# Optimization experiments

Hardware: AMD Instinct MI355X
Metric: run time of the kernel (lower is better)

## Reference

```python
import jax, jax.numpy as jnp
import numpy as np

B = 16          # number of point clouds in the batch
PTS = 32768     # points per cloud (lengths sum to N)
N = B * PTS     # total stacked points
D = 512         # feature dim


def setup_inputs() -> dict:
    key = jax.random.key(0)
    k_feat, = jax.random.split(key, 1)
    features = jax.random.normal(k_feat, (N, D), dtype=jnp.float32)
    # per-cloud point counts; must sum to N (static). Equal lengths here,
    # but reference() handles arbitrary ragged lengths.
    stack_lengths = jnp.full((B,), PTS, dtype=jnp.int32)
    return {"stack_lengths": stack_lengths, "features": features}


def reference(stack_lengths, features):
    # Ragged per-segment mean pooling: features [N, D] -> [B, D]
    n_points = features.shape[0]
    batch = stack_lengths.shape[0]
    # segment id for every point; total_repeat_length keeps shapes static under jit
    seg_ids = jnp.repeat(jnp.arange(batch), stack_lengths,
                         total_repeat_length=n_points)
    sums = jax.ops.segment_sum(features, seg_ids, num_segments=batch)  # [B, D]
    counts = stack_lengths.astype(features.dtype)[:, None]             # [B, 1]
    return sums / counts
```

## Files before the change

kernel.cpp:

```cpp
#include <hip/hip_runtime.h>


#define SPLIT 256
#define TPB   128

__global__ void zero_out_kernel(float* __restrict__ out, int n) {
    int i = blockIdx.x * blockDim.x + threadIdx.x;
    if (i < n) out[i] = 0.0f;
}

__global__ __launch_bounds__(TPB) void seg_mean_kernel(
        const int* __restrict__ lens,
        const float* __restrict__ feat,
        float* __restrict__ out,
        int B) {
    const int D = 512;
    const int seg   = blockIdx.x / SPLIT;
    const int split = blockIdx.x % SPLIT;

    long long start = 0;
    for (int b = 0; b < seg; ++b) start += lens[b];
    const int len = lens[seg];

    const int col = threadIdx.x * 4;
    const float* base = feat + start * (long long)D + col;

    float4 acc = make_float4(0.f, 0.f, 0.f, 0.f);
    for (int r = split; r < len; r += SPLIT) {
        float4 v = *(const float4*)(base + (long long)r * D);
        acc.x += v.x; acc.y += v.y; acc.z += v.z; acc.w += v.w;
    }

    const float inv = (len > 0) ? (1.0f / (float)len) : 0.0f;
    float* o = out + (long long)seg * D + col;
    atomicAdd(o + 0, acc.x * inv);
    atomicAdd(o + 1, acc.y * inv);
    atomicAdd(o + 2, acc.z * inv);
    atomicAdd(o + 3, acc.w * inv);
}

extern "C" void kernel_launch(void* const* d_in, const int* in_sizes, int n_in,
                              void* d_out, int out_size, void* d_ws, size_t ws_size,
                              hipStream_t stream) {
    const int*   lens = (const int*)d_in[0];
    const float* feat = (const float*)d_in[1];
    float*       out  = (float*)d_out;
    const int B = in_sizes[0];

    zero_out_kernel<<<(out_size + 255) / 256, 256, 0, stream>>>(out, out_size);

    seg_mean_kernel<<<B * SPLIT, TPB, 0, stream>>>(lens, feat, out, B);
}
```

Measured before the change: 1.313 ms.

## Use contiguous row chunks per block with 4-way unrolled accumulation

Each block now sums a contiguous run of rows instead of a strided interleave across the segment, so it reads one sequential span of memory. The inner loop is unrolled by four with independent accumulators, keeping more loads in flight per thread. The zeroing kernel is replaced with hipMemsetAsync, and blocks with no rows skip their atomics. Summation order changes slightly, which can shift floating-point rounding.

```diff
diff --git a/kernel.cpp b/kernel.cpp
--- a/kernel.cpp
+++ b/kernel.cpp
@@ -4,16 +4,10 @@
 #define SPLIT 256
 #define TPB   128
 
-__global__ void zero_out_kernel(float* __restrict__ out, int n) {
-    int i = blockIdx.x * blockDim.x + threadIdx.x;
-    if (i < n) out[i] = 0.0f;
-}
-
 __global__ __launch_bounds__(TPB) void seg_mean_kernel(
         const int* __restrict__ lens,
         const float* __restrict__ feat,
-        float* __restrict__ out,
-        int B) {
+        float* __restrict__ out) {
     const int D = 512;
     const int seg   = blockIdx.x / SPLIT;
     const int split = blockIdx.x % SPLIT;
@@ -22,21 +16,46 @@
     for (int b = 0; b < seg; ++b) start += lens[b];
     const int len = lens[seg];
 
+    const int chunk = (len + SPLIT - 1) / SPLIT;
+    const int r0 = split * chunk;
+    const int r1 = (r0 + chunk < len) ? (r0 + chunk) : len;
+    const int nrows = r1 - r0;
+
     const int col = threadIdx.x * 4;
-    const float* base = feat + start * (long long)D + col;
+    const float* base = feat + (start + (long long)r0) * D + col;
 
-    float4 acc = make_float4(0.f, 0.f, 0.f, 0.f);
-    for (int r = split; r < len; r += SPLIT) {
+    float4 a0 = make_float4(0.f, 0.f, 0.f, 0.f);
+    float4 a1 = a0, a2 = a0, a3 = a0;
+
+    int r = 0;
+    for (; r + 4 <= nrows; r += 4) {
+        float4 v0 = *(const float4*)(base + (long long)(r + 0) * D);
+        float4 v1 = *(const float4*)(base + (long long)(r + 1) * D);
+        float4 v2 = *(const float4*)(base + (long long)(r + 2) * D);
+        float4 v3 = *(const float4*)(base + (long long)(r + 3) * D);
+        a0.x += v0.x; a0.y += v0.y; a0.z += v0.z; a0.w += v0.w;
+        a1.x += v1.x; a1.y += v1.y; a1.z += v1.z; a1.w += v1.w;
+        a2.x += v2.x; a2.y += v2.y; a2.z += v2.z; a2.w += v2.w;
+        a3.x += v3.x; a3.y += v3.y; a3.z += v3.z; a3.w += v3.w;
+    }
+    for (; r < nrows; ++r) {
         float4 v = *(const float4*)(base + (long long)r * D);
-        acc.x += v.x; acc.y += v.y; acc.z += v.z; acc.w += v.w;
+        a0.x += v.x; a0.y += v.y; a0.z += v.z; a0.w += v.w;
     }
+
+    a0.x += a1.x + a2.x + a3.x;
+    a0.y += a1.y + a2.y + a3.y;
+    a0.z += a1.z + a2.z + a3.z;
+    a0.w += a1.w + a2.w + a3.w;
 
     const float inv = (len > 0) ? (1.0f / (float)len) : 0.0f;
     float* o = out + (long long)seg * D + col;
-    atomicAdd(o + 0, acc.x * inv);
-    atomicAdd(o + 1, acc.y * inv);
-    atomicAdd(o + 2, acc.z * inv);
-    atomicAdd(o + 3, acc.w * inv);
+    if (nrows > 0) {
+        atomicAdd(o + 0, a0.x * inv);
+        atomicAdd(o + 1, a0.y * inv);
+        atomicAdd(o + 2, a0.z * inv);
+        atomicAdd(o + 3, a0.w * inv);
+    }
 }
 
 extern "C" void kernel_launch(void* const* d_in, const int* in_sizes, int n_in,
@@ -47,7 +66,7 @@
     float*       out  = (float*)d_out;
     const int B = in_sizes[0];
 
-    zero_out_kernel<<<(out_size + 255) / 256, 256, 0, stream>>>(out, out_size);
+    hipMemsetAsync(out, 0, (size_t)out_size * sizeof(float), stream);
 
-    seg_mean_kernel<<<B * SPLIT, TPB, 0, stream>>>(lens, feat, out, B);
+    seg_mean_kernel<<<B * SPLIT, TPB, 0, stream>>>(lens, feat, out);
 }
```

Result: no change. 1.328 ms (+1.1%).
